# Kernel tuning notes

Hardware: AMD Instinct MI355X
Metric: run time of the kernel (lower is better)

The kernel has to match this reference:

```python
import jax, jax.numpy as jnp
import numpy as np

N_EMBD = 1024
N_HEAD = 16
HEAD_DIM = N_EMBD // N_HEAD
WINDOW = 256


def setup_inputs() -> dict:
    key = jax.random.key(0)
    ks = jax.random.split(key, 9)
    B, T, C = 2, 2048, N_EMBD
    s = 1.0 / np.sqrt(C)
    inp = {
        'x': jax.random.normal(ks[0], (B, T, C), jnp.float32),
        'Wq': jax.random.normal(ks[1], (C, C), jnp.float32) * s,
        'bq': jnp.zeros((C,), jnp.float32),
        'Wk': jax.random.normal(ks[2], (C, C), jnp.float32) * s,
        'bk': jnp.zeros((C,), jnp.float32),
        'Wv': jax.random.normal(ks[3], (C, C), jnp.float32) * s,
        'bv': jnp.zeros((C,), jnp.float32),
        'Wo': jax.random.normal(ks[4], (C, C), jnp.float32) * s,
        'bo': jnp.zeros((C,), jnp.float32),
    }
    return inp


def reference(x, Wq, bq, Wk, bk, Wv, bv, Wo, bo):
    B, T, C = x.shape
    H, D = N_HEAD, HEAD_DIM
    # projections -> [B, H, T, D]
    q = (x @ Wq + bq).reshape(B, T, H, D).transpose(0, 2, 1, 3)
    k = (x @ Wk + bk).reshape(B, T, H, D).transpose(0, 2, 1, 3)
    v = (x @ Wv + bv).reshape(B, T, H, D).transpose(0, 2, 1, 3)
    # dense scores [B, H, T, T]
    scores = jnp.einsum('bhid,bhjd->bhij', q, k) / jnp.sqrt(jnp.float32(D))
    # sliding-window + causal mask: allow j <= i and i - j <= WINDOW
    i = jnp.arange(T)[:, None]
    j = jnp.arange(T)[None, :]
    mask = (j <= i) & (i - j <= WINDOW)  # [T, T]
    scores = jnp.where(mask[None, None], scores, -jnp.inf)
    probs = jax.nn.softmax(scores, axis=-1)
    out = jnp.einsum('bhij,bhjd->bhid', probs, v)  # [B,H,T,D]
    out = out.transpose(0, 2, 1, 3).reshape(B, T, C)
    return out @ Wo + bo
```

## Files before the change

### kernel.cpp

```cpp
#include <hip/hip_runtime.h>


typedef _Float16 f16;
typedef _Float16 half8 __attribute__((ext_vector_type(8)));
typedef _Float16 half4 __attribute__((ext_vector_type(4)));
typedef float    f32x4 __attribute__((ext_vector_type(4)));

#define MFMA16(a, b, c) __builtin_amdgcn_mfma_f32_16x16x32_f16((a), (b), (c), 0, 0, 0)

__device__ __forceinline__ void gload16(const void* g, void* l) {
  __builtin_amdgcn_global_load_lds(
      (const __attribute__((address_space(1))) void*)g,
      (__attribute__((address_space(3))) void*)l, 16, 0, 0);
}

__global__ __launch_bounds__(256) void prep_kernel(
    const float* __restrict__ x, f16* __restrict__ xb,
    const float* __restrict__ W0, const float* __restrict__ W1,
    const float* __restrict__ W2, const float* __restrict__ W3,
    f16* __restrict__ T0, f16* __restrict__ T1,
    f16* __restrict__ T2, f16* __restrict__ T3) {
  const int bid = blockIdx.x;
  if (bid < 2048) {
    const int idx = (bid * 256 + threadIdx.x) * 8;
    const float4 a = *(const float4*)(x + idx);
    const float4 b = *(const float4*)(x + idx + 4);
    half8 h;
    h[0] = (f16)a.x; h[1] = (f16)a.y; h[2] = (f16)a.z; h[3] = (f16)a.w;
    h[4] = (f16)b.x; h[5] = (f16)b.y; h[6] = (f16)b.z; h[7] = (f16)b.w;
    *(half8*)(xb + idx) = h;
    return;
  }
  __shared__ float tile[32][33];
  const int rem0 = bid - 2048;
  const int mat = rem0 >> 10;
  const int rem = rem0 & 1023;
  const int kt = (rem >> 5) * 32;
  const int nt = (rem & 31) * 32;
  const float* W = mat == 0 ? W0 : mat == 1 ? W1 : mat == 2 ? W2 : W3;
  f16* T = mat == 0 ? T0 : mat == 1 ? T1 : mat == 2 ? T2 : T3;
  const int tid = threadIdx.x;
  const int r = tid >> 3;
  const int c4 = (tid & 7) * 4;
  const float4 v = *(const float4*)(W + (size_t)(kt + r) * 1024 + nt + c4);
  tile[r][c4 + 0] = v.x; tile[r][c4 + 1] = v.y;
  tile[r][c4 + 2] = v.z; tile[r][c4 + 3] = v.w;
  __syncthreads();
  half4 o;
  #pragma unroll
  for (int e = 0; e < 4; e++) o[e] = (f16)tile[c4 + e][r];
  *(half4*)(T + (size_t)(nt + r) * 1024 + kt + c4) = o;
}

__device__ __forceinline__ void gemm_core4(const f16* __restrict__ A,
                                           const f16* __restrict__ Bt,
                                           int m0, int n0,
                                           f16* As, f16* Bs,
                                           f32x4 acc[4][4]) {
  const int tid = threadIdx.x;
  const int lane = tid & 63, wave = tid >> 6;
  const int wm = wave >> 1, wn = wave & 1;
  const int fr = lane & 15, fg = lane >> 4;
  const int sx = (fr & 7) << 4;

  const int srow = wave * 32 + (lane >> 3);
  const int cc = lane & 7;
  const size_t go = (size_t)srow * 1024 + (size_t)((cc ^ (srow & 7)) * 8);
  const f16* ag = A + (size_t)m0 * 1024 + go;
  const f16* bg = Bt + (size_t)n0 * 1024 + go;
  f16* la = As + wave * 2048;
  f16* lb = Bs + wave * 2048;

  #pragma unroll
  for (int i = 0; i < 4; i++)
    #pragma unroll
    for (int j = 0; j < 4; j++) acc[i][j] = (f32x4){0.f, 0.f, 0.f, 0.f};

  for (int kt = 0; kt < 1024; kt += 64) {
    #pragma unroll
    for (int t = 0; t < 4; t++) {
      gload16(ag + kt + t * 8192, la + t * 512);
      gload16(bg + kt + t * 8192, lb + t * 512);
    }
    __syncthreads();
    const char* Ab = (const char*)As;
    const char* Bb = (const char*)Bs;
    #pragma unroll
    for (int kk = 0; kk < 2; kk++) {
      half8 af[4], bf[4];
      const int co = (kk * 64 + fg * 16) ^ sx;
      #pragma unroll
      for (int mf = 0; mf < 4; mf++)
        af[mf] = *(const half8*)(Ab + (wm * 64 + mf * 16 + fr) * 128 + co);
      #pragma unroll
      for (int nf = 0; nf < 4; nf++)
        bf[nf] = *(const half8*)(Bb + (wn * 64 + nf * 16 + fr) * 128 + co);
      #pragma unroll
      for (int mf = 0; mf < 4; mf++)
        #pragma unroll
        for (int nf = 0; nf < 4; nf++)
          acc[mf][nf] = MFMA16(af[mf], bf[nf], acc[mf][nf]);
    }
    __syncthreads();
  }
}

__global__ __launch_bounds__(256, 3) void gemm_qkv_kernel(
    const f16* __restrict__ xb, const f16* __restrict__ wt,
    const float* __restrict__ bq, const float* __restrict__ bk,
    const float* __restrict__ bv,
    f16* __restrict__ qo, f16* __restrict__ ko, f16* __restrict__ vt) {
  __shared__ __align__(16) f16 As[128 * 64];
  __shared__ __align__(16) f16 Bs[128 * 64];
  const int wg = (blockIdx.x & 7) * 96 + (blockIdx.x >> 3);
  const int m0 = (wg & 31) * 128;
  const int n0 = (wg >> 5) * 128;
  f32x4 acc[4][4];
  gemm_core4(xb, wt, m0, n0, As, Bs, acc);

  const int lane = threadIdx.x & 63, wave = threadIdx.x >> 6;
  const int wm = wave >> 1, wn = wave & 1;
  const int fr = lane & 15, fg = lane >> 4;
  const int matid = n0 >> 10;
  const int nc0 = n0 & 1023;
  const float* bias = matid == 0 ? bq : matid == 1 ? bk : bv;
  if (matid < 2) {
    f16* out = matid == 0 ? qo : ko;
    #pragma unroll
    for (int mf = 0; mf < 4; mf++)
      #pragma unroll
      for (int nf = 0; nf < 4; nf++) {
        const int col = nc0 + wn * 64 + nf * 16 + fr;
        const float bb = bias[col];
        #pragma unroll
        for (int r = 0; r < 4; r++) {
          const int row = m0 + wm * 64 + mf * 16 + fg * 4 + r;
          out[(size_t)row * 1024 + col] = (f16)(acc[mf][nf][r] + bb);
        }
      }
  } else {
    #pragma unroll
    for (int mf = 0; mf < 4; mf++)
      #pragma unroll
      for (int nf = 0; nf < 4; nf++) {
        const int row = m0 + wm * 64 + mf * 16 + fg * 4;
        const int col = nc0 + wn * 64 + nf * 16 + fr;
        const int b = row >> 11, t = row & 2047;
        const int h = col >> 6, d = col & 63;
        const float bb = bias[col];
        half4 vv;
        #pragma unroll
        for (int r = 0; r < 4; r++) vv[r] = (f16)(acc[mf][nf][r] + bb);
        *(half4*)(vt + (((size_t)(b * 16 + h)) * 64 + d) * 2048 + t) = vv;
      }
  }
}

__device__ __forceinline__ void gemm_core8(const f16* __restrict__ A,
                                           const f16* __restrict__ Bt,
                                           int m0, int n0,
                                           f16* As, f16* Bs,
                                           f32x4 acc[4][2]) {
  const int tid = threadIdx.x;
  const int lane = tid & 63, wave = tid >> 6;
  const int wm = wave >> 2, wn = wave & 3;
  const int fr = lane & 15, fg = lane >> 4;

  const int srow = wave * 16 + (lane >> 3);
  const int cc = lane & 7;
  const size_t go = (size_t)srow * 1024 + (size_t)((cc ^ (srow & 7)) * 8);
  const f16* ag = A + (size_t)m0 * 1024 + go;
  const f16* bg = Bt + (size_t)n0 * 1024 + go;
  f16* la = As + wave * 1024;
  f16* lb = Bs + wave * 1024;

  #pragma unroll
  for (int i = 0; i < 4; i++)
    #pragma unroll
    for (int j = 0; j < 2; j++) acc[i][j] = (f32x4){0.f, 0.f, 0.f, 0.f};

  for (int kt = 0; kt < 1024; kt += 64) {
    gload16(ag + kt, la);
    gload16(ag + kt + 8192, la + 512);
    gload16(bg + kt, lb);
    gload16(bg + kt + 8192, lb + 512);
    __syncthreads();
    const char* Ab = (const char*)As;
    const char* Bb = (const char*)Bs;
    half8 af[4][2], bf[2][2];
    #pragma unroll
    for (int mf = 0; mf < 4; mf++) {
      const int row = wm * 64 + mf * 16 + fr;
      const int sw = (row & 7) << 4;
      #pragma unroll
      for (int kk = 0; kk < 2; kk++)
        af[mf][kk] = *(const half8*)(Ab + row * 128 + ((kk * 64 + fg * 16) ^ sw));
    }
    #pragma unroll
    for (int nf = 0; nf < 2; nf++) {
      const int row = wn * 32 + nf * 16 + fr;
      const int sw = (row & 7) << 4;
      #pragma unroll
      for (int kk = 0; kk < 2; kk++)
        bf[nf][kk] = *(const half8*)(Bb + row * 128 + ((kk * 64 + fg * 16) ^ sw));
    }
    #pragma unroll
    for (int mf = 0; mf < 4; mf++)
      #pragma unroll
      for (int nf = 0; nf < 2; nf++)
        #pragma unroll
        for (int kk = 0; kk < 2; kk++)
          acc[mf][nf] = MFMA16(af[mf][kk], bf[nf][kk], acc[mf][nf]);
    __syncthreads();
  }
}

__global__ __launch_bounds__(512, 4) void gemm_o_kernel(
    const f16* __restrict__ ao, const f16* __restrict__ wot,
    const float* __restrict__ bo, float* __restrict__ out) {
  __shared__ __align__(16) f16 As[128 * 64];
  __shared__ __align__(16) f16 Bs[128 * 64];
  const int wg = (blockIdx.x & 7) * 32 + (blockIdx.x >> 3);
  const int m0 = (wg & 31) * 128;
  const int n0 = (wg >> 5) * 128;
  f32x4 acc[4][2];
  gemm_core8(ao, wot, m0, n0, As, Bs, acc);

  const int lane = threadIdx.x & 63, wave = threadIdx.x >> 6;
  const int wm = wave >> 2, wn = wave & 3;
  const int fr = lane & 15, fg = lane >> 4;
  #pragma unroll
  for (int mf = 0; mf < 4; mf++)
    #pragma unroll
    for (int nf = 0; nf < 2; nf++) {
      const int col = n0 + wn * 32 + nf * 16 + fr;
      const float bb = bo[col];
      #pragma unroll
      for (int r = 0; r < 4; r++) {
        const int row = m0 + wm * 64 + mf * 16 + fg * 4 + r;
        out[(size_t)row * 1024 + col] = acc[mf][nf][r] + bb;
      }
    }
}

__global__ __launch_bounds__(256, 3) void attn_kernel(
    const f16* __restrict__ Q, const f16* __restrict__ K,
    const f16* __restrict__ Vt, f16* __restrict__ Ao) {
  __shared__ __align__(16) f16 Ks[2][64 * 64];
  __shared__ __align__(16) f16 Vs[2][64 * 64];
  __shared__ __align__(16) f16 Ps[4][16][72];

  const int tid = threadIdx.x, lane = tid & 63, wave = tid >> 6;
  const int fr = lane & 15, g = lane >> 4;
  const int qt = blockIdx.x & 31, bh = blockIdx.x >> 5;
  const int b = bh >> 4, h = bh & 15;
  const int q0 = qt * 64;
  const int qr = q0 + wave * 16;

  const f16* Qb = Q + ((size_t)(b * 2048 + qr)) * 1024 + h * 64;
  const half8 q0f = *(const half8*)(Qb + (size_t)fr * 1024 + g * 8);
  const half8 q1f = *(const half8*)(Qb + (size_t)fr * 1024 + 32 + g * 8);

  const char* Kg = (const char*)(K + ((size_t)(b * 2048)) * 1024 + h * 64);
  const char* Vg = (const char*)(Vt + ((size_t)(b * 16 + h)) * 64 * 2048);

  const int sr0 = wave * 16 + (lane >> 3);
  const int sr1 = sr0 + 8;
  const int sc = lane & 7;
  const int sco0 = (sc ^ (sr0 & 7)) << 4;
  const int sco1 = (sc ^ (sr1 & 7)) << 4;

  auto stageKV = [&](int buf, int jt) {
    gload16(Kg + (size_t)(jt + sr0) * 2048 + sco0, (f16*)Ks[buf] + wave * 1024);
    gload16(Kg + (size_t)(jt + sr1) * 2048 + sco1,
            (f16*)Ks[buf] + wave * 1024 + 512);
    gload16(Vg + (size_t)sr0 * 4096 + (size_t)jt * 2 + sco0,
            (f16*)Vs[buf] + wave * 1024);
    gload16(Vg + (size_t)sr1 * 4096 + (size_t)jt * 2 + sco1,
            (f16*)Vs[buf] + wave * 1024 + 512);
  };

  const int t0 = qt >= 4 ? qt - 4 : 0;
  const int t1 = qt;

  f32x4 O[4];
  #pragma unroll
  for (int nt = 0; nt < 4; nt++) O[nt] = (f32x4){0.f, 0.f, 0.f, 0.f};
  float lsum[4] = {0.f, 0.f, 0.f, 0.f};

  stageKV(0, t0 * 64);
  __syncthreads();

  for (int tt = t0; tt <= t1; ++tt) {
    const int cur = (tt - t0) & 1;
    if (tt < t1) stageKV(cur ^ 1, (tt + 1) * 64);
    const int jt = tt * 64;
    const bool alive = (jt <= qr + 15) && (jt + 63 >= qr - 256);
    if (alive) {
      const char* Kb = (const char*)Ks[cur];
      const char* Vb = (const char*)Vs[cur];
      f32x4 s[4];
      #pragma unroll
      for (int jj = 0; jj < 4; ++jj) {
        const int kj = jj * 16 + fr;
        const char* krow = Kb + kj * 128;
        const int kswz = (kj & 7) << 4;
        const half8 kf0 = *(const half8*)(krow + ((g * 16) ^ kswz));
        const half8 kf1 = *(const half8*)(krow + ((64 + g * 16) ^ kswz));
        s[jj] = (f32x4){0.f, 0.f, 0.f, 0.f};
        s[jj] = MFMA16(q0f, kf0, s[jj]);
        s[jj] = MFMA16(q1f, kf1, s[jj]);
      }
      const int eb0 = qr + g * 4 - jt - fr;
      #pragma unroll
      for (int jj = 0; jj < 4; ++jj) {
        #pragma unroll
        for (int r = 0; r < 4; ++r) {
          const float a = __expf(s[jj][r] * 0.125f - 3.0f);
          const float p = ((unsigned)(eb0 + r - jj * 16) <= 256u) ? a : 0.f;
          lsum[r] += p;
          Ps[wave][g * 4 + r][jj * 16 + fr] = (f16)p;
        }
      }
      #pragma unroll
      for (int ks = 0; ks < 2; ++ks) {
        const half8 pa = *(const half8*)(&Ps[wave][fr][ks * 32 + g * 8]);
        #pragma unroll
        for (int nt = 0; nt < 4; ++nt) {
          const int vd = nt * 16 + fr;
          const half8 vf = *(const half8*)(
              Vb + vd * 128 + ((ks * 64 + g * 16) ^ ((vd & 7) << 4)));
          O[nt] = MFMA16(pa, vf, O[nt]);
        }
      }
    }
    __syncthreads();
  }

  float inv[4];
  #pragma unroll
  for (int r = 0; r < 4; ++r) {
    float s = lsum[r];
    s += __shfl_xor(s, 1);
    s += __shfl_xor(s, 2);
    s += __shfl_xor(s, 4);
    s += __shfl_xor(s, 8);
    inv[r] = 1.0f / s;
  }
  f16* Aout = Ao + ((size_t)(b * 2048 + qr)) * 1024 + h * 64;
  #pragma unroll
  for (int nt = 0; nt < 4; ++nt)
    #pragma unroll
    for (int r = 0; r < 4; ++r)
      Aout[(size_t)(g * 4 + r) * 1024 + nt * 16 + fr] =
          (f16)(O[nt][r] * inv[r]);
}

extern "C" void kernel_launch(void* const* d_in, const int* in_sizes, int n_in,
                              void* d_out, int out_size, void* d_ws,
                              size_t ws_size, hipStream_t stream) {
  const float* x  = (const float*)d_in[0];
  const float* Wq = (const float*)d_in[1];
  const float* bq = (const float*)d_in[2];
  const float* Wk = (const float*)d_in[3];
  const float* bk = (const float*)d_in[4];
  const float* Wv = (const float*)d_in[5];
  const float* bv = (const float*)d_in[6];
  const float* Wo = (const float*)d_in[7];
  const float* bo = (const float*)d_in[8];

  char* w = (char*)d_ws;
  f16* xb  = (f16*)(w);
  f16* wqt = (f16*)(w + ((size_t)8 << 20));
  f16* wkt = (f16*)(w + ((size_t)10 << 20));
  f16* wvt = (f16*)(w + ((size_t)12 << 20));
  f16* wot = (f16*)(w + ((size_t)14 << 20));
  f16* q   = (f16*)(w + ((size_t)16 << 20));
  f16* kk  = (f16*)(w + ((size_t)24 << 20));
  f16* vt  = (f16*)(w + ((size_t)32 << 20));
  f16* ao  = (f16*)(w + ((size_t)40 << 20));

  prep_kernel<<<6144, 256, 0, stream>>>(x, xb, Wq, Wk, Wv, Wo,
                                        wqt, wkt, wvt, wot);
  gemm_qkv_kernel<<<768, 256, 0, stream>>>(xb, wqt, bq, bk, bv, q, kk, vt);
  attn_kernel<<<1024, 256, 0, stream>>>(q, kk, vt, ao);
  gemm_o_kernel<<<256, 512, 0, stream>>>(ao, wot, bo, (float*)d_out);
}
```

Baseline: 83.92 us.

## Enlarge attention query tile to 128 rows and retile output GEMM

Result: faster. 80.06 us (-4.6%).

```diff
diff --git a/kernel.cpp b/kernel.cpp
--- a/kernel.cpp
+++ b/kernel.cpp
@@ -156,79 +156,64 @@
   }
 }
 
-__device__ __forceinline__ void gemm_core8(const f16* __restrict__ A,
-                                           const f16* __restrict__ Bt,
-                                           int m0, int n0,
-                                           f16* As, f16* Bs,
-                                           f32x4 acc[4][2]) {
-  const int tid = threadIdx.x;
-  const int lane = tid & 63, wave = tid >> 6;
-  const int wm = wave >> 2, wn = wave & 3;
-  const int fr = lane & 15, fg = lane >> 4;
-
-  const int srow = wave * 16 + (lane >> 3);
-  const int cc = lane & 7;
-  const size_t go = (size_t)srow * 1024 + (size_t)((cc ^ (srow & 7)) * 8);
-  const f16* ag = A + (size_t)m0 * 1024 + go;
-  const f16* bg = Bt + (size_t)n0 * 1024 + go;
-  f16* la = As + wave * 1024;
-  f16* lb = Bs + wave * 1024;
-
-  #pragma unroll
-  for (int i = 0; i < 4; i++)
-    #pragma unroll
-    for (int j = 0; j < 2; j++) acc[i][j] = (f32x4){0.f, 0.f, 0.f, 0.f};
-
-  for (int kt = 0; kt < 1024; kt += 64) {
-    gload16(ag + kt, la);
-    gload16(ag + kt + 8192, la + 512);
-    gload16(bg + kt, lb);
-    gload16(bg + kt + 8192, lb + 512);
-    __syncthreads();
-    const char* Ab = (const char*)As;
-    const char* Bb = (const char*)Bs;
-    half8 af[4][2], bf[2][2];
-    #pragma unroll
-    for (int mf = 0; mf < 4; mf++) {
-      const int row = wm * 64 + mf * 16 + fr;
-      const int sw = (row & 7) << 4;
-      #pragma unroll
-      for (int kk = 0; kk < 2; kk++)
-        af[mf][kk] = *(const half8*)(Ab + row * 128 + ((kk * 64 + fg * 16) ^ sw));
-    }
-    #pragma unroll
-    for (int nf = 0; nf < 2; nf++) {
-      const int row = wn * 32 + nf * 16 + fr;
-      const int sw = (row & 7) << 4;
-      #pragma unroll
-      for (int kk = 0; kk < 2; kk++)
-        bf[nf][kk] = *(const half8*)(Bb + row * 128 + ((kk * 64 + fg * 16) ^ sw));
-    }
-    #pragma unroll
-    for (int mf = 0; mf < 4; mf++)
-      #pragma unroll
-      for (int nf = 0; nf < 2; nf++)
-        #pragma unroll
-        for (int kk = 0; kk < 2; kk++)
-          acc[mf][nf] = MFMA16(af[mf][kk], bf[nf][kk], acc[mf][nf]);
-    __syncthreads();
-  }
-}
-
-__global__ __launch_bounds__(512, 4) void gemm_o_kernel(
+__global__ __launch_bounds__(256, 4) void gemm_o_kernel(
     const f16* __restrict__ ao, const f16* __restrict__ wot,
     const float* __restrict__ bo, float* __restrict__ out) {
   __shared__ __align__(16) f16 As[128 * 64];
-  __shared__ __align__(16) f16 Bs[128 * 64];
-  const int wg = (blockIdx.x & 7) * 32 + (blockIdx.x >> 3);
+  __shared__ __align__(16) f16 Bs[64 * 64];
+  const int wg = (blockIdx.x & 7) * 64 + (blockIdx.x >> 3);
   const int m0 = (wg & 31) * 128;
-  const int n0 = (wg >> 5) * 128;
+  const int n0 = (wg >> 5) * 64;
+
+  const int tid = threadIdx.x;
+  const int lane = tid & 63, wave = tid >> 6;
+  const int wm = wave >> 1, wn = wave & 1;
+  const int fr = lane & 15, fg = lane >> 4;
+  const int sx = (fr & 7) << 4;
+
+  const int cc = lane & 7;
+  const int srA = wave * 32 + (lane >> 3);
+  const int srB = wave * 16 + (lane >> 3);
+  const size_t goA = (size_t)srA * 1024 + (size_t)((cc ^ (srA & 7)) * 8);
+  const size_t goB = (size_t)srB * 1024 + (size_t)((cc ^ (srB & 7)) * 8);
+  const f16* ag = ao + (size_t)m0 * 1024 + goA;
+  const f16* bg = wot + (size_t)n0 * 1024 + goB;
+  f16* la = As + wave * 2048;
+  f16* lb = Bs + wave * 1024;
+
   f32x4 acc[4][2];
-  gemm_core8(ao, wot, m0, n0, As, Bs, acc);
-
-  const int lane = threadIdx.x & 63, wave = threadIdx.x >> 6;
-  const int wm = wave >> 2, wn = wave & 3;
-  const int fr = lane & 15, fg = lane >> 4;
+  #pragma unroll
+  for (int i = 0; i < 4; i++)
+    #pragma unroll
+    for (int j = 0; j < 2; j++) acc[i][j] = (f32x4){0.f, 0.f, 0.f, 0.f};
+
+  for (int kt = 0; kt < 1024; kt += 64) {
+    #pragma unroll
+    for (int t = 0; t < 4; t++) gload16(ag + kt + t * 8192, la + t * 512);
+    #pragma unroll
+    for (int t = 0; t < 2; t++) gload16(bg + kt + t * 8192, lb + t * 512);
+    __syncthreads();
+    const char* Ab = (const char*)As;
+    const char* Bb = (const char*)Bs;
+    #pragma unroll
+    for (int kk = 0; kk < 2; kk++) {
+      half8 af[4], bf[2];
+      const int co = (kk * 64 + fg * 16) ^ sx;
+      #pragma unroll
+      for (int mf = 0; mf < 4; mf++)
+        af[mf] = *(const half8*)(Ab + (wm * 64 + mf * 16 + fr) * 128 + co);
+      #pragma unroll
+      for (int nf = 0; nf < 2; nf++)
+        bf[nf] = *(const half8*)(Bb + (wn * 32 + nf * 16 + fr) * 128 + co);
+      #pragma unroll
+      for (int mf = 0; mf < 4; mf++)
+        #pragma unroll
+        for (int nf = 0; nf < 2; nf++)
+          acc[mf][nf] = MFMA16(af[mf], bf[nf], acc[mf][nf]);
+    }
+    __syncthreads();
+  }
+
   #pragma unroll
   for (int mf = 0; mf < 4; mf++)
     #pragma unroll
@@ -248,45 +233,49 @@
     const f16* __restrict__ Vt, f16* __restrict__ Ao) {
   __shared__ __align__(16) f16 Ks[2][64 * 64];
   __shared__ __align__(16) f16 Vs[2][64 * 64];
-  __shared__ __align__(16) f16 Ps[4][16][72];
+  __shared__ __align__(16) f16 Ps[4][32][72];
 
   const int tid = threadIdx.x, lane = tid & 63, wave = tid >> 6;
   const int fr = lane & 15, g = lane >> 4;
-  const int qt = blockIdx.x & 31, bh = blockIdx.x >> 5;
+  const int qt = blockIdx.x & 15, bh = blockIdx.x >> 4;
   const int b = bh >> 4, h = bh & 15;
-  const int q0 = qt * 64;
-  const int qr = q0 + wave * 16;
+  const int q0 = qt * 128;
+  const int qr = q0 + wave * 32;
 
   const f16* Qb = Q + ((size_t)(b * 2048 + qr)) * 1024 + h * 64;
-  const half8 q0f = *(const half8*)(Qb + (size_t)fr * 1024 + g * 8);
-  const half8 q1f = *(const half8*)(Qb + (size_t)fr * 1024 + 32 + g * 8);
+  half8 qf[2][2];
+  #pragma unroll
+  for (int mc = 0; mc < 2; mc++)
+    #pragma unroll
+    for (int kk = 0; kk < 2; kk++)
+      qf[mc][kk] =
+          *(const half8*)(Qb + (size_t)(mc * 16 + fr) * 1024 + kk * 32 + g * 8);
 
   const char* Kg = (const char*)(K + ((size_t)(b * 2048)) * 1024 + h * 64);
   const char* Vg = (const char*)(Vt + ((size_t)(b * 16 + h)) * 64 * 2048);
 
-  const int sr0 = wave * 16 + (lane >> 3);
-  const int sr1 = sr0 + 8;
-  const int sc = lane & 7;
-  const int sco0 = (sc ^ (sr0 & 7)) << 4;
-  const int sco1 = (sc ^ (sr1 & 7)) << 4;
+  const int sr = wave * 16 + (lane >> 3);
+  const int sco = ((lane & 7) ^ (sr & 7)) << 4;
 
   auto stageKV = [&](int buf, int jt) {
-    gload16(Kg + (size_t)(jt + sr0) * 2048 + sco0, (f16*)Ks[buf] + wave * 1024);
-    gload16(Kg + (size_t)(jt + sr1) * 2048 + sco1,
-            (f16*)Ks[buf] + wave * 1024 + 512);
-    gload16(Vg + (size_t)sr0 * 4096 + (size_t)jt * 2 + sco0,
-            (f16*)Vs[buf] + wave * 1024);
-    gload16(Vg + (size_t)sr1 * 4096 + (size_t)jt * 2 + sco1,
-            (f16*)Vs[buf] + wave * 1024 + 512);
+    #pragma unroll
+    for (int t = 0; t < 2; t++) {
+      gload16(Kg + (size_t)(jt + sr + t * 8) * 2048 + sco,
+              (f16*)Ks[buf] + wave * 1024 + t * 512);
+      gload16(Vg + (size_t)(sr + t * 8) * 4096 + (size_t)jt * 2 + sco,
+              (f16*)Vs[buf] + wave * 1024 + t * 512);
+    }
   };
 
-  const int t0 = qt >= 4 ? qt - 4 : 0;
-  const int t1 = qt;
-
-  f32x4 O[4];
-  #pragma unroll
-  for (int nt = 0; nt < 4; nt++) O[nt] = (f32x4){0.f, 0.f, 0.f, 0.f};
-  float lsum[4] = {0.f, 0.f, 0.f, 0.f};
+  const int t0 = q0 >= 256 ? (q0 - 256) >> 6 : 0;
+  const int t1 = (q0 + 127) >> 6;
+
+  f32x4 O[2][4];
+  #pragma unroll
+  for (int mc = 0; mc < 2; mc++)
+    #pragma unroll
+    for (int nt = 0; nt < 4; nt++) O[mc][nt] = (f32x4){0.f, 0.f, 0.f, 0.f};
+  float lsum[2][4] = {{0.f, 0.f, 0.f, 0.f}, {0.f, 0.f, 0.f, 0.f}};
 
   stageKV(0, t0 * 64);
   __syncthreads();
@@ -295,11 +284,11 @@
     const int cur = (tt - t0) & 1;
     if (tt < t1) stageKV(cur ^ 1, (tt + 1) * 64);
     const int jt = tt * 64;
-    const bool alive = (jt <= qr + 15) && (jt + 63 >= qr - 256);
+    const bool alive = (jt <= qr + 31) && (jt + 63 >= qr - 256);
     if (alive) {
       const char* Kb = (const char*)Ks[cur];
       const char* Vb = (const char*)Vs[cur];
-      f32x4 s[4];
+      f32x4 s[2][4];
       #pragma unroll
       for (int jj = 0; jj < 4; ++jj) {
         const int kj = jj * 16 + fr;
@@ -307,53 +296,66 @@
         const int kswz = (kj & 7) << 4;
         const half8 kf0 = *(const half8*)(krow + ((g * 16) ^ kswz));
         const half8 kf1 = *(const half8*)(krow + ((64 + g * 16) ^ kswz));
-        s[jj] = (f32x4){0.f, 0.f, 0.f, 0.f};
-        s[jj] = MFMA16(q0f, kf0, s[jj]);
-        s[jj] = MFMA16(q1f, kf1, s[jj]);
-      }
-      const int eb0 = qr + g * 4 - jt - fr;
-      #pragma unroll
-      for (int jj = 0; jj < 4; ++jj) {
-        #pragma unroll
-        for (int r = 0; r < 4; ++r) {
-          const float a = __expf(s[jj][r] * 0.125f - 3.0f);
-          const float p = ((unsigned)(eb0 + r - jj * 16) <= 256u) ? a : 0.f;
-          lsum[r] += p;
-          Ps[wave][g * 4 + r][jj * 16 + fr] = (f16)p;
+        #pragma unroll
+        for (int mc = 0; mc < 2; mc++) {
+          f32x4 z = (f32x4){0.f, 0.f, 0.f, 0.f};
+          z = MFMA16(qf[mc][0], kf0, z);
+          z = MFMA16(qf[mc][1], kf1, z);
+          s[mc][jj] = z;
         }
       }
       #pragma unroll
+      for (int mc = 0; mc < 2; mc++) {
+        const int eb = qr + mc * 16 + g * 4 - jt - fr;
+        #pragma unroll
+        for (int jj = 0; jj < 4; ++jj) {
+          #pragma unroll
+          for (int r = 0; r < 4; ++r) {
+            const float a = __expf(s[mc][jj][r] * 0.125f - 3.0f);
+            const float p = ((unsigned)(eb + r - jj * 16) <= 256u) ? a : 0.f;
+            lsum[mc][r] += p;
+            Ps[wave][mc * 16 + g * 4 + r][jj * 16 + fr] = (f16)p;
+          }
+        }
+      }
+      #pragma unroll
       for (int ks = 0; ks < 2; ++ks) {
-        const half8 pa = *(const half8*)(&Ps[wave][fr][ks * 32 + g * 8]);
+        const half8 pa0 = *(const half8*)(&Ps[wave][fr][ks * 32 + g * 8]);
+        const half8 pa1 = *(const half8*)(&Ps[wave][16 + fr][ks * 32 + g * 8]);
         #pragma unroll
         for (int nt = 0; nt < 4; ++nt) {
           const int vd = nt * 16 + fr;
           const half8 vf = *(const half8*)(
               Vb + vd * 128 + ((ks * 64 + g * 16) ^ ((vd & 7) << 4)));
-          O[nt] = MFMA16(pa, vf, O[nt]);
+          O[0][nt] = MFMA16(pa0, vf, O[0][nt]);
+          O[1][nt] = MFMA16(pa1, vf, O[1][nt]);
         }
       }
     }
     __syncthreads();
   }
 
-  float inv[4];
-  #pragma unroll
-  for (int r = 0; r < 4; ++r) {
-    float s = lsum[r];
-    s += __shfl_xor(s, 1);
-    s += __shfl_xor(s, 2);
-    s += __shfl_xor(s, 4);
-    s += __shfl_xor(s, 8);
-    inv[r] = 1.0f / s;
-  }
+  float inv[2][4];
+  #pragma unroll
+  for (int mc = 0; mc < 2; mc++)
+    #pragma unroll
+    for (int r = 0; r < 4; ++r) {
+      float s = lsum[mc][r];
+      s += __shfl_xor(s, 1);
+      s += __shfl_xor(s, 2);
+      s += __shfl_xor(s, 4);
+      s += __shfl_xor(s, 8);
+      inv[mc][r] = 1.0f / s;
+    }
   f16* Aout = Ao + ((size_t)(b * 2048 + qr)) * 1024 + h * 64;
   #pragma unroll
-  for (int nt = 0; nt < 4; ++nt)
-    #pragma unroll
-    for (int r = 0; r < 4; ++r)
-      Aout[(size_t)(g * 4 + r) * 1024 + nt * 16 + fr] =
-          (f16)(O[nt][r] * inv[r]);
+  for (int mc = 0; mc < 2; mc++)
+    #pragma unroll
+    for (int nt = 0; nt < 4; ++nt)
+      #pragma unroll
+      for (int r = 0; r < 4; ++r)
+        Aout[(size_t)(mc * 16 + g * 4 + r) * 1024 + nt * 16 + fr] =
+            (f16)(O[mc][nt][r] * inv[mc][r]);
 }
 
 extern "C" void kernel_launch(void* const* d_in, const int* in_sizes, int n_in,
@@ -383,6 +385,6 @@
   prep_kernel<<<6144, 256, 0, stream>>>(x, xb, Wq, Wk, Wv, Wo,
                                         wqt, wkt, wvt, wot);
   gemm_qkv_kernel<<<768, 256, 0, stream>>>(xb, wqt, bq, bk, bv, q, kk, vt);
-  attn_kernel<<<1024, 256, 0, stream>>>(q, kk, vt, ao);
-  gemm_o_kernel<<<256, 512, 0, stream>>>(ao, wot, bo, (float*)d_out);
-}
+  attn_kernel<<<512, 256, 0, stream>>>(q, kk, vt, ao);
+  gemm_o_kernel<<<512, 256, 0, stream>>>(ao, wot, bo, (float*)d_out);
+}
```
